# Performance work log

Measured on AMD Instinct MI355X. Metric: run time of the kernel, lower is better.

The kernel has to match this reference:

```python
import jax, jax.numpy as jnp
import numpy as np

N_NODES = 10000

def rgcn_layer(x, edge_index, basis, comp, root, bias):
    # x: [N, Fin]; edge_index: [R, 2, E] int; basis: [B, Fin, Fout]; comp: [R, B]
    R, _, E = edge_index.shape
    N = x.shape[0]
    src = edge_index[:, 0]  # [R, E]
    dst = edge_index[:, 1]  # [R, E]
    # basis-decomposed per-relation weights: W_r = sum_b comp[r,b] * basis[b]
    W = jnp.einsum('rb,bio->rio', comp, basis)          # [R, Fin, Fout]
    x_src = x[src]                                       # [R, E, Fin] gather
    msg = jnp.einsum('rei,rio->reo', x_src, W)           # [R, E, Fout]
    # per-relation mean aggregation onto destination nodes
    seg = (jnp.arange(R, dtype=dst.dtype)[:, None] * N + dst).reshape(-1)  # [R*E]
    agg = jax.ops.segment_sum(msg.reshape(R * E, -1), seg, num_segments=R * N)
    deg = jax.ops.segment_sum(jnp.ones((R * E,), x.dtype), seg, num_segments=R * N)
    agg = agg / jnp.maximum(deg, 1.0)[:, None]
    agg = agg.reshape(R, N, -1).sum(0)                   # sum over relations
    return agg + x @ root + bias


def setup_inputs() -> dict:
    key = jax.random.key(0)
    ks = jax.random.split(key, 10)
    s = 0.05  # scale params for numerical sanity
    return {
        'x_drug': jax.random.normal(ks[0], (N_NODES, 2048), jnp.float32),
        'drug_w': jax.random.normal(ks[1], (2048, 128), jnp.float32) * s,
        'edge_index': jax.random.randint(ks[2], (100, 2, 5000), 0, N_NODES, jnp.int32),
        'basis1': jax.random.normal(ks[3], (8, 128, 64), jnp.float32) * s,
        'comp1': jax.random.normal(ks[4], (100, 8), jnp.float32) * s,
        'root1': jax.random.normal(ks[5], (128, 64), jnp.float32) * s,
        'bias1': jnp.zeros((64,), jnp.float32),
        'basis2': jax.random.normal(ks[6], (8, 64, 20), jnp.float32) * s,
        'comp2': jax.random.normal(ks[7], (100, 8), jnp.float32) * s,
        'root2': jax.random.normal(ks[8], (64, 20), jnp.float32) * s,
        'bias2': jnp.zeros((20,), jnp.float32),
    }


def reference(x_drug, drug_w, edge_index, basis1, comp1, root1, bias1,
              basis2, comp2, root2, bias2):
    x = x_drug @ drug_w                                   # dense projection [N, 128]
    h = rgcn_layer(x, edge_index, basis1, comp1, root1, bias1)   # [N, 64]
    h = jax.nn.relu(h)
    out = rgcn_layer(h, edge_index, basis2, comp2, root2, bias2)  # [N, 20]
    return out
```

## Files before the change

### kernel.cpp

```cpp
#include <hip/hip_runtime.h>

#define NN 10000
#define RR 100
#define EE 5000
#define D0 2048
#define D1 128
#define D2 64
#define D3 20
#define NE (RR*EE)
#define MAXD 128

using short8  = __attribute__((ext_vector_type(8))) short;
using float4e = __attribute__((ext_vector_type(4))) float;

typedef const __attribute__((address_space(1))) void g_void;
typedef __attribute__((address_space(3))) void l_void;

__device__ __forceinline__ unsigned short f2bf(float f) {
  unsigned int u = __float_as_uint(f);
  unsigned int r = u + 0x7fffu + ((u >> 16) & 1u);
  return (unsigned short)(r >> 16);
}
__device__ __forceinline__ float bf2f(unsigned short u) {
  return __uint_as_float(((unsigned int)u) << 16);
}
__device__ __forceinline__ unsigned int pk2(float lo, float hi) {
  return ((unsigned int)f2bf(hi) << 16) | (unsigned int)f2bf(lo);
}

#define ZBLK 977
#define CURB 10
#define WTBLK 1024
#define W1BLK 288
#define W2BLK 72
__global__ __launch_bounds__(256) void prep_kernel(
    const float* __restrict__ W, const float* __restrict__ root1,
    const float* __restrict__ basis1, const float* __restrict__ root2,
    const float* __restrict__ basis2, int4* __restrict__ deg4,
    int4* __restrict__ cur4,
    unsigned short* __restrict__ Btw, unsigned short* __restrict__ Wc1T,
    unsigned short* __restrict__ Wc2T) {
  const int b = blockIdx.x, tid = threadIdx.x;
  if (b < ZBLK) {
    int i = b * 256 + tid;
    if (i < (NN * RR) / 4) deg4[i] = make_int4(0, 0, 0, 0);
  } else if (b < ZBLK + CURB) {
    int i = (b - ZBLK) * 256 + tid;
    if (i < 2504) cur4[i] = make_int4(0, 0, 0, 0);
  } else if (b < ZBLK + CURB + WTBLK) {
    int idx = (b - ZBLK - CURB) * 256 + tid;
    int n = idx >> 11, k = idx & 2047;
    Btw[idx] = f2bf(W[(size_t)k * 128 + n]);
  } else if (b < ZBLK + CURB + WTBLK + W1BLK) {
    int idx = (b - ZBLK - CURB - WTBLK) * 256 + tid;
    int o = idx / 1152, j = idx - o * 1152;
    float v = (j < 128) ? root1[j * 64 + o] : basis1[(j - 128) * 64 + o];
    Wc1T[idx] = f2bf(v);
  } else {
    int idx = (b - ZBLK - CURB - WTBLK - W1BLK) * 256 + tid;
    int c = idx / 576, j = idx - c * 576;
    float v = 0.f;
    if (c < 20) v = (j < 64) ? root2[j * 20 + c] : basis2[(j - 64) * 20 + c];
    Wc2T[idx] = f2bf(v);
  }
}

__global__ void deg_kernel(const int* __restrict__ ei, int* __restrict__ deg) {
  int gid = blockIdx.x * 256 + threadIdx.x;
  if (gid >= NE) return;
  int r = gid / EE, e = gid - r * EE;
  int d = ei[r * 2 * EE + EE + e];
  atomicAdd(&deg[r * NN + d], 1);
}

__global__ void scatter_kernel(const int* __restrict__ ei,
                               const int* __restrict__ deg,
                               int* __restrict__ cur, int* __restrict__ rec,
                               float* __restrict__ esc) {
  int gid = blockIdx.x * 256 + threadIdx.x;
  if (gid >= NE) return;
  int r = gid / EE, e = gid - r * EE;
  int s = ei[r * 2 * EE + e];
  int d = ei[r * 2 * EE + EE + e];
  int p = atomicAdd(&cur[d], 1);
  if (p < MAXD) {
    rec[d * MAXD + p] = (r << 14) | s;
    esc[d * MAXD + p] = 1.0f / fmaxf((float)deg[r * NN + d], 1.0f);
  }
}

__global__ __launch_bounds__(256) void gemm0_mfma(
    const float* __restrict__ A, const unsigned short* __restrict__ Btw,
    float* __restrict__ xp) {
  __shared__ __align__(16) unsigned short Asb[2][32 * 64];
  __shared__ __align__(16) unsigned short Bsb[2][128 * 64];
  const int tid = threadIdx.x;
  const int m0 = blockIdx.x * 32;
  const int ks = blockIdx.y;
  const int wv = tid >> 6, lane = tid & 63;
  const int lrow = lane & 15, quad = lane >> 4;
  const int mt = wv >> 1;
  const int nh = (wv & 1) * 4;

  const int ar = tid >> 3, ag = tid & 7;
  int gra = m0 + ar; if (gra >= NN) gra = NN - 1;
  const float* Ap = &A[(size_t)gra * D0 + ks * 512 + ag * 4];
  const int asw = (ar & 7) << 4;
  const int aw0 = (ar * 128 + ((ag * 8) ^ asw)) >> 1;
  const int aw1 = (ar * 128 + ((64 + ag * 8) ^ asw)) >> 1;

  const int rowB = wv * 32 + (lane >> 3);
  const int gch  = (lane & 7) ^ (lane >> 3);
  const unsigned short* BgBase = &Btw[(size_t)rowB * D0 + ks * 512 + gch * 8];
  const int ldsB = wv * 2048;

  float4 a0, a1;

#define G0_LOADB(buf, c)                                                     \
  { _Pragma("unroll")                                                        \
    for (int i = 0; i < 4; i++) {                                            \
      __builtin_amdgcn_global_load_lds(                                      \
          (g_void*)(BgBase + (size_t)i * 8 * D0 + (c) * 64),                 \
          (l_void*)&Bsb[buf][ldsB + i * 512], 16, 0, 0);                     \
    } }

#define G0_LOADA(c)                                  \
  { a0 = *(const float4*)(Ap + (c) * 64);            \
    a1 = *(const float4*)(Ap + (c) * 64 + 32); }

#define G0_STOREA(buf)                                                  \
  { uint2 p0, p1;                                                       \
    p0.x = pk2(a0.x, a0.y); p0.y = pk2(a0.z, a0.w);                     \
    p1.x = pk2(a1.x, a1.y); p1.y = pk2(a1.z, a1.w);                     \
    *(uint2*)&Asb[buf][aw0] = p0;                                       \
    *(uint2*)&Asb[buf][aw1] = p1; }

#define G0_COMPUTE(buf)                                                 \
  { const int arow = mt * 16 + lrow;                                    \
    const int aswz = (arow & 7) << 4;                                   \
    _Pragma("unroll")                                                   \
    for (int kk = 0; kk < 2; kk++) {                                    \
      short8 af = *(const short8*)&Asb[buf][(arow * 128 + ((quad * 16 + kk * 64) ^ aswz)) >> 1]; \
      _Pragma("unroll")                                                 \
      for (int nt = 0; nt < 4; nt++) {                                  \
        const int brow = (nh + nt) * 16 + lrow;                         \
        short8 bfr = *(const short8*)&Bsb[buf][(brow * 128 + ((quad * 16 + kk * 64) ^ ((brow & 7) << 4))) >> 1]; \
        acc[nt] = __builtin_amdgcn_mfma_f32_16x16x32_bf16(af, bfr, acc[nt], 0, 0, 0); \
      }                                                                 \
    } }

  float4e acc[4];
#pragma unroll
  for (int i = 0; i < 4; i++) { acc[i][0]=0.f; acc[i][1]=0.f; acc[i][2]=0.f; acc[i][3]=0.f; }

  G0_LOADB(0, 0);
  G0_LOADA(0);
  G0_STOREA(0);
  __syncthreads();

#pragma unroll
  for (int c = 0; c < 8; c++) {
    if (c < 7) {
      G0_LOADB((c + 1) & 1, c + 1);
      G0_LOADA(c + 1);
      __builtin_amdgcn_sched_barrier(0);
    }
    G0_COMPUTE(c & 1);
    if (c < 7) G0_STOREA((c + 1) & 1);
    __syncthreads();
  }

#pragma unroll
  for (int nt = 0; nt < 4; nt++) {
    const int col = (nh + nt) * 16 + lrow;
#pragma unroll
    for (int r = 0; r < 4; r++) {
      const int row = m0 + mt * 16 + quad * 4 + r;
      if (row < NN)
        xp[(size_t)ks * (NN * D1) + (size_t)row * D1 + col] = acc[nt][r];
    }
  }
}

__global__ void reduce_kernel(const float* __restrict__ xp,
                              unsigned short* __restrict__ xb) {
  int idx = (blockIdx.x * 256 + threadIdx.x) * 4;
  if (idx >= NN * D1) return;
  float4 a = *(const float4*)&xp[idx];
  float4 b = *(const float4*)&xp[NN * D1 + idx];
  float4 c = *(const float4*)&xp[2 * NN * D1 + idx];
  float4 d = *(const float4*)&xp[3 * NN * D1 + idx];
  ushort4 o;
  o.x = f2bf(a.x + b.x + c.x + d.x); o.y = f2bf(a.y + b.y + c.y + d.y);
  o.z = f2bf(a.z + b.z + c.z + d.z); o.w = f2bf(a.w + b.w + c.w + d.w);
  *(ushort4*)&xb[idx] = o;
}

__global__ __launch_bounds__(256) void agg1e_kernel(
    const unsigned short* __restrict__ xb, const int* __restrict__ cur,
    const int* __restrict__ rec, const float* __restrict__ esc,
    const float* __restrict__ comp, unsigned short* __restrict__ A1b) {
  __shared__ float s_comp[RR * 8];
  const int tid = threadIdx.x;
  for (int i = tid; i < RR * 8; i += 256) s_comp[i] = comp[i];
  __syncthreads();
  const int wv = tid >> 6, lane = tid & 63;
  const int n = blockIdx.x * 4 + wv;
  if (n >= NN) return;
  float acc[8][2];
#pragma unroll
  for (int b = 0; b < 8; b++) { acc[b][0] = 0.f; acc[b][1] = 0.f; }
  int cnt = cur[n]; if (cnt > MAXD) cnt = MAXD;
  const int beg = n * MAXD, end = beg + cnt;
  int idx = beg;
  for (; idx + 3 < end; idx += 4) {
    int rc[4]; float sc[4]; unsigned int xv[4];
#pragma unroll
    for (int u = 0; u < 4; u++) {
      rc[u] = rec[idx + u];
      sc[u] = esc[idx + u];
    }
#pragma unroll
    for (int u = 0; u < 4; u++)
      xv[u] = *(const unsigned int*)&xb[(size_t)(rc[u] & 16383) * D1 + lane * 2];
#pragma unroll
    for (int u = 0; u < 4; u++) {
      const float* cb = &s_comp[(rc[u] >> 14) * 8];
      float x0 = __uint_as_float((xv[u] & 0xffffu) << 16);
      float x1 = __uint_as_float(xv[u] & 0xffff0000u);
#pragma unroll
      for (int b = 0; b < 8; b++) {
        float w = sc[u] * cb[b];
        acc[b][0] += w * x0;
        acc[b][1] += w * x1;
      }
    }
  }
  for (; idx < end; idx++) {
    int rc = rec[idx];
    float sc = esc[idx];
    unsigned int xv = *(const unsigned int*)&xb[(size_t)(rc & 16383) * D1 + lane * 2];
    const float* cb = &s_comp[(rc >> 14) * 8];
    float x0 = __uint_as_float((xv & 0xffffu) << 16);
    float x1 = __uint_as_float(xv & 0xffff0000u);
#pragma unroll
    for (int b = 0; b < 8; b++) {
      float w = sc * cb[b];
      acc[b][0] += w * x0;
      acc[b][1] += w * x1;
    }
  }
#pragma unroll
  for (int b = 0; b < 8; b++) {
    ushort2 o; o.x = f2bf(acc[b][0]); o.y = f2bf(acc[b][1]);
    *(ushort2*)&A1b[(size_t)n * 1024 + b * 128 + lane * 2] = o;
  }
}

__global__ __launch_bounds__(256) void agg2e_kernel(
    const unsigned short* __restrict__ hb, const int* __restrict__ cur,
    const int* __restrict__ rec, const float* __restrict__ esc,
    const float* __restrict__ comp, unsigned short* __restrict__ A2b) {
  __shared__ float s_comp[RR * 8];
  const int tid = threadIdx.x;
  for (int i = tid; i < RR * 8; i += 256) s_comp[i] = comp[i];
  __syncthreads();
  const int wv = tid >> 6, lane = tid & 63;
  const int n = blockIdx.x * 4 + wv;
  if (n >= NN) return;
  float acc[8];
#pragma unroll
  for (int b = 0; b < 8; b++) acc[b] = 0.f;
  int cnt = cur[n]; if (cnt > MAXD) cnt = MAXD;
  const int beg = n * MAXD, end = beg + cnt;
  int idx = beg;
  for (; idx + 3 < end; idx += 4) {
    int rc[4]; float sc[4]; float hv[4];
#pragma unroll
    for (int u = 0; u < 4; u++) {
      rc[u] = rec[idx + u];
      sc[u] = esc[idx + u];
    }
#pragma unroll
    for (int u = 0; u < 4; u++)
      hv[u] = bf2f(hb[(size_t)(rc[u] & 16383) * D2 + lane]);
#pragma unroll
    for (int u = 0; u < 4; u++) {
      const float* cb = &s_comp[(rc[u] >> 14) * 8];
#pragma unroll
      for (int b = 0; b < 8; b++) acc[b] += sc[u] * cb[b] * hv[u];
    }
  }
  for (; idx < end; idx++) {
    int rc = rec[idx];
    float sc = esc[idx];
    float hv = bf2f(hb[(size_t)(rc & 16383) * D2 + lane]);
    const float* cb = &s_comp[(rc >> 14) * 8];
#pragma unroll
    for (int b = 0; b < 8; b++) acc[b] += sc * cb[b] * hv;
  }
#pragma unroll
  for (int b = 0; b < 8; b++)
    A2b[(size_t)n * 512 + b * 64 + lane] = f2bf(acc[b]);
}

__global__ __launch_bounds__(256) void hlayer_mfma(
    const unsigned short* __restrict__ xb, const unsigned short* __restrict__ A1b,
    const unsigned short* __restrict__ Wt, const float* __restrict__ bias1,
    unsigned short* __restrict__ hb) {
  __shared__ __align__(16) unsigned short Asb[2][32 * 64];
  __shared__ __align__(16) unsigned short Bsb[2][64 * 64];
  const int tid = threadIdx.x;
  const int m0 = blockIdx.x * 32;
  const int wv = tid >> 6, lane = tid & 63;
  const int lrow = lane & 15, quad = lane >> 4;
  const int mt = wv >> 1, nb = wv & 1;

  const int ar = tid >> 3, ac = tid & 7;
  int gr = m0 + ar; if (gr >= NN) gr = NN - 1;
  const unsigned short* Ax = &xb[(size_t)gr * D1 + ac * 8];
  const unsigned short* Aa = &A1b[(size_t)gr * 1024 + ac * 8];
  const int asw = (ar & 7) << 4;
  const int aw = (ar * 128 + ((ac * 16) ^ asw)) >> 1;

  const int br = tid >> 2, bq = tid & 3;
  const unsigned short* Bp = &Wt[(size_t)br * 1152 + bq * 16];
  const int bsw = (br & 7) << 4;
  const int bw0 = (br * 128 + ((bq * 32) ^ bsw)) >> 1;
  const int bw1 = (br * 128 + ((bq * 32 + 16) ^ bsw)) >> 1;

  uint4 ra, rb0, rb1;

#define H_LOADG(c)                                                       \
  { int kb = (c) * 64;                                                   \
    ra  = (kb < 128) ? *(const uint4*)(Ax + kb)                          \
                     : *(const uint4*)(Aa + (kb - 128));                 \
    rb0 = *(const uint4*)(Bp + kb);                                      \
    rb1 = *(const uint4*)(Bp + kb + 8); }

#define H_STOREL(buf)                                                    \
  { *(uint4*)&Asb[buf][aw]  = ra;                                        \
    *(uint4*)&Bsb[buf][bw0] = rb0;                                       \
    *(uint4*)&Bsb[buf][bw1] = rb1; }

#define H_COMPUTE(buf)                                                   \
  { const int arow = mt * 16 + lrow;                                     \
    const int aswz = (arow & 7) << 4;                                    \
    _Pragma("unroll")                                                    \
    for (int kk = 0; kk < 2; kk++) {                                     \
      short8 af = *(const short8*)&Asb[buf][(arow * 128 + ((quad * 16 + kk * 64) ^ aswz)) >> 1]; \
      _Pragma("unroll")                                                  \
      for (int nt = 0; nt < 2; nt++) {                                   \
        const int brow = nb * 32 + nt * 16 + lrow;                       \
        short8 bfr = *(const short8*)&Bsb[buf][(brow * 128 + ((quad * 16 + kk * 64) ^ ((brow & 7) << 4))) >> 1]; \
        acc[nt] = __builtin_amdgcn_mfma_f32_16x16x32_bf16(af, bfr, acc[nt], 0, 0, 0); \
      }                                                                  \
    } }

  float4e acc[2];
#pragma unroll
  for (int i = 0; i < 2; i++) { acc[i][0]=0.f; acc[i][1]=0.f; acc[i][2]=0.f; acc[i][3]=0.f; }

  H_LOADG(0);
  H_STOREL(0);
  __syncthreads();

#pragma unroll
  for (int c = 0; c < 18; c++) {
    if (c < 17) {
      H_LOADG(c + 1);
      __builtin_amdgcn_sched_barrier(0);
    }
    H_COMPUTE(c & 1);
    if (c < 17) H_STOREL((c + 1) & 1);
    __syncthreads();
  }

#pragma unroll
  for (int nt = 0; nt < 2; nt++) {
    int col = nb * 32 + nt * 16 + lrow;
    float bv = bias1[col];
#pragma unroll
    for (int r = 0; r < 4; r++) {
      int row = m0 + mt * 16 + quad * 4 + r;
      if (row < NN)
        hb[(size_t)row * D2 + col] = f2bf(fmaxf(acc[nt][r] + bv, 0.f));
    }
  }
}

__global__ __launch_bounds__(256) void out_mfma(
    const unsigned short* __restrict__ hb, const unsigned short* __restrict__ A2b,
    const unsigned short* __restrict__ Wt, const float* __restrict__ bias2,
    float* __restrict__ out) {
  __shared__ __align__(16) unsigned short Asb[2][32 * 64];
  __shared__ __align__(16) unsigned short Bsb[2][32 * 64];
  const int tid = threadIdx.x;
  const int m0 = blockIdx.x * 32;
  const int wv = tid >> 6, lane = tid & 63;
  const int lrow = lane & 15, quad = lane >> 4;
  const int mt = wv >> 1, ntn = wv & 1;

  const int ar = tid >> 3, ac = tid & 7;
  int gr = m0 + ar; if (gr >= NN) gr = NN - 1;
  const unsigned short* Ah = &hb[(size_t)gr * D2 + ac * 8];
  const unsigned short* Aa = &A2b[(size_t)gr * 512 + ac * 8];
  const unsigned short* Bp = &Wt[(size_t)ar * 576 + ac * 8];
  const int asw = (ar & 7) << 4;
  const int aw = (ar * 128 + ((ac * 16) ^ asw)) >> 1;

  uint4 ra, rb;

#define O_LOADG(c)                                                       \
  { int kb = (c) * 64;                                                   \
    ra = (kb < 64) ? *(const uint4*)(Ah)                                 \
                   : *(const uint4*)(Aa + (kb - 64));                    \
    rb = *(const uint4*)(Bp + kb); }

#define O_STOREL(buf)                                                    \
  { *(uint4*)&Asb[buf][aw] = ra;                                         \
    *(uint4*)&Bsb[buf][aw] = rb; }

#define O_COMPUTE(buf)                                                   \
  { const int arow = mt * 16 + lrow;                                     \
    const int aswz = (arow & 7) << 4;                                    \
    const int brow = ntn * 16 + lrow;                                    \
    const int bswz = (brow & 7) << 4;                                    \
    _Pragma("unroll")                                                    \
    for (int kk = 0; kk < 2; kk++) {                                     \
      short8 af = *(const short8*)&Asb[buf][(arow * 128 + ((quad * 16 + kk * 64) ^ aswz)) >> 1]; \
      short8 bfr = *(const short8*)&Bsb[buf][(brow * 128 + ((quad * 16 + kk * 64) ^ bswz)) >> 1]; \
      acc = __builtin_amdgcn_mfma_f32_16x16x32_bf16(af, bfr, acc, 0, 0, 0); \
    } }

  float4e acc;
  acc[0]=0.f; acc[1]=0.f; acc[2]=0.f; acc[3]=0.f;

  O_LOADG(0);
  O_STOREL(0);
  __syncthreads();

#pragma unroll
  for (int c = 0; c < 9; c++) {
    if (c < 8) {
      O_LOADG(c + 1);
      __builtin_amdgcn_sched_barrier(0);
    }
    O_COMPUTE(c & 1);
    if (c < 8) O_STOREL((c + 1) & 1);
    __syncthreads();
  }

  int col = ntn * 16 + lrow;
  if (col < D3) {
    float bv = bias2[col];
#pragma unroll
    for (int r = 0; r < 4; r++) {
      int row = m0 + mt * 16 + quad * 4 + r;
      if (row < NN)
        out[(size_t)row * D3 + col] = acc[r] + bv;
    }
  }
}

extern "C" void kernel_launch(void* const* d_in, const int* in_sizes, int n_in,
                              void* d_out, int out_size, void* d_ws,
                              size_t ws_size, hipStream_t stream) {
  const float* x_drug = (const float*)d_in[0];
  const float* drug_w = (const float*)d_in[1];
  const int*   ei     = (const int*)d_in[2];
  const float* basis1 = (const float*)d_in[3];
  const float* comp1  = (const float*)d_in[4];
  const float* root1  = (const float*)d_in[5];
  const float* bias1  = (const float*)d_in[6];
  const float* basis2 = (const float*)d_in[7];
  const float* comp2  = (const float*)d_in[8];
  const float* root2  = (const float*)d_in[9];
  const float* bias2  = (const float*)d_in[10];
  float* out = (float*)d_out;

  float* ws = (float*)d_ws;
  int*   deg  = (int*)ws;
  int*   cur  = deg + 1000000;
  int*   rec  = cur + 10016;
  float* esc  = (float*)(rec + NN * MAXD);
  unsigned short* xb   = (unsigned short*)(esc + NN * MAXD);
  unsigned short* hb   = (unsigned short*)((float*)xb + 640000);
  unsigned short* Btw  = (unsigned short*)((float*)hb + 320000);
  unsigned short* Wc1T = (unsigned short*)((float*)Btw + 131072);
  unsigned short* Wc2T = (unsigned short*)((float*)Wc1T + 36864);
  float* R1 = (float*)Wc2T + 9216;
  float* xp = R1;
  unsigned short* A1b = (unsigned short*)R1;
  unsigned short* A2b = (unsigned short*)R1;

  prep_kernel<<<ZBLK + CURB + WTBLK + W1BLK + W2BLK, 256, 0, stream>>>(
      drug_w, root1, basis1, root2, basis2, (int4*)deg, (int4*)cur,
      Btw, Wc1T, Wc2T);

  deg_kernel<<<(NE + 255) / 256, 256, 0, stream>>>(ei, deg);
  scatter_kernel<<<(NE + 255) / 256, 256, 0, stream>>>(ei, deg, cur, rec, esc);

  gemm0_mfma<<<dim3(313, 4), 256, 0, stream>>>(x_drug, Btw, xp);
  reduce_kernel<<<(NN * D1 / 4 + 255) / 256, 256, 0, stream>>>(xp, xb);

  agg1e_kernel<<<(NN + 3) / 4, 256, 0, stream>>>(xb, cur, rec, esc, comp1, A1b);
  hlayer_mfma<<<(NN + 31) / 32, 256, 0, stream>>>(xb, A1b, Wc1T, bias1, hb);

  agg2e_kernel<<<(NN + 3) / 4, 256, 0, stream>>>(hb, cur, rec, esc, comp2, A2b);
  out_mfma<<<(NN + 31) / 32, 256, 0, stream>>>(hb, A2b, Wc2T, bias2, out);
}
```

Baseline: 174.6 us.

## Drop split-K in input projection GEMM and write bf16 directly

```diff
diff --git a/kernel.cpp b/kernel.cpp
--- a/kernel.cpp
+++ b/kernel.cpp
@@ -91,30 +91,24 @@
 
 __global__ __launch_bounds__(256) void gemm0_mfma(
     const float* __restrict__ A, const unsigned short* __restrict__ Btw,
-    float* __restrict__ xp) {
-  __shared__ __align__(16) unsigned short Asb[2][32 * 64];
+    unsigned short* __restrict__ xb) {
+  __shared__ __align__(16) unsigned short Asb[2][16 * 64];
   __shared__ __align__(16) unsigned short Bsb[2][128 * 64];
   const int tid = threadIdx.x;
-  const int m0 = blockIdx.x * 32;
-  const int ks = blockIdx.y;
+  const int m0 = blockIdx.x * 16;
   const int wv = tid >> 6, lane = tid & 63;
   const int lrow = lane & 15, quad = lane >> 4;
-  const int mt = wv >> 1;
-  const int nh = (wv & 1) * 4;
-
-  const int ar = tid >> 3, ag = tid & 7;
-  int gra = m0 + ar; if (gra >= NN) gra = NN - 1;
-  const float* Ap = &A[(size_t)gra * D0 + ks * 512 + ag * 4];
-  const int asw = (ar & 7) << 4;
-  const int aw0 = (ar * 128 + ((ag * 8) ^ asw)) >> 1;
-  const int aw1 = (ar * 128 + ((64 + ag * 8) ^ asw)) >> 1;
+
+  const int ar = tid >> 4, ag = tid & 15;
+  const float* Ap = &A[(size_t)(m0 + ar) * D0 + ag * 4];
+  const int aw = (ar * 128 + ((ag * 8) ^ ((ar & 7) << 4))) >> 1;
 
   const int rowB = wv * 32 + (lane >> 3);
   const int gch  = (lane & 7) ^ (lane >> 3);
-  const unsigned short* BgBase = &Btw[(size_t)rowB * D0 + ks * 512 + gch * 8];
+  const unsigned short* BgBase = &Btw[(size_t)rowB * D0 + gch * 8];
   const int ldsB = wv * 2048;
 
-  float4 a0, a1;
+  float4 a0;
 
 #define G0_LOADB(buf, c)                                                     \
   { _Pragma("unroll")                                                        \
@@ -124,76 +118,56 @@
           (l_void*)&Bsb[buf][ldsB + i * 512], 16, 0, 0);                     \
     } }
 
-#define G0_LOADA(c)                                  \
-  { a0 = *(const float4*)(Ap + (c) * 64);            \
-    a1 = *(const float4*)(Ap + (c) * 64 + 32); }
+#define G0_LOADA(c)  { a0 = *(const float4*)(Ap + (c) * 64); }
 
 #define G0_STOREA(buf)                                                  \
-  { uint2 p0, p1;                                                       \
+  { uint2 p0;                                                           \
     p0.x = pk2(a0.x, a0.y); p0.y = pk2(a0.z, a0.w);                     \
-    p1.x = pk2(a1.x, a1.y); p1.y = pk2(a1.z, a1.w);                     \
-    *(uint2*)&Asb[buf][aw0] = p0;                                       \
-    *(uint2*)&Asb[buf][aw1] = p1; }
+    *(uint2*)&Asb[buf][aw] = p0; }
 
 #define G0_COMPUTE(buf)                                                 \
-  { const int arow = mt * 16 + lrow;                                    \
-    const int aswz = (arow & 7) << 4;                                   \
+  { const int aswz = (lrow & 7) << 4;                                   \
     _Pragma("unroll")                                                   \
     for (int kk = 0; kk < 2; kk++) {                                    \
-      short8 af = *(const short8*)&Asb[buf][(arow * 128 + ((quad * 16 + kk * 64) ^ aswz)) >> 1]; \
+      short8 af = *(const short8*)&Asb[buf][(lrow * 128 + ((quad * 16 + kk * 64) ^ aswz)) >> 1]; \
       _Pragma("unroll")                                                 \
-      for (int nt = 0; nt < 4; nt++) {                                  \
-        const int brow = (nh + nt) * 16 + lrow;                         \
+      for (int nt = 0; nt < 2; nt++) {                                  \
+        const int brow = wv * 32 + nt * 16 + lrow;                      \
         short8 bfr = *(const short8*)&Bsb[buf][(brow * 128 + ((quad * 16 + kk * 64) ^ ((brow & 7) << 4))) >> 1]; \
         acc[nt] = __builtin_amdgcn_mfma_f32_16x16x32_bf16(af, bfr, acc[nt], 0, 0, 0); \
       }                                                                 \
     } }
 
-  float4e acc[4];
-#pragma unroll
-  for (int i = 0; i < 4; i++) { acc[i][0]=0.f; acc[i][1]=0.f; acc[i][2]=0.f; acc[i][3]=0.f; }
+  float4e acc[2];
+#pragma unroll
+  for (int i = 0; i < 2; i++) { acc[i][0]=0.f; acc[i][1]=0.f; acc[i][2]=0.f; acc[i][3]=0.f; }
 
   G0_LOADB(0, 0);
   G0_LOADA(0);
   G0_STOREA(0);
   __syncthreads();
 
-#pragma unroll
-  for (int c = 0; c < 8; c++) {
-    if (c < 7) {
+#pragma unroll 4
+  for (int c = 0; c < 32; c++) {
+    if (c < 31) {
       G0_LOADB((c + 1) & 1, c + 1);
       G0_LOADA(c + 1);
       __builtin_amdgcn_sched_barrier(0);
     }
     G0_COMPUTE(c & 1);
-    if (c < 7) G0_STOREA((c + 1) & 1);
+    if (c < 31) G0_STOREA((c + 1) & 1);
     __syncthreads();
   }
 
 #pragma unroll
-  for (int nt = 0; nt < 4; nt++) {
-    const int col = (nh + nt) * 16 + lrow;
+  for (int nt = 0; nt < 2; nt++) {
+    const int col = wv * 32 + nt * 16 + lrow;
 #pragma unroll
     for (int r = 0; r < 4; r++) {
-      const int row = m0 + mt * 16 + quad * 4 + r;
-      if (row < NN)
-        xp[(size_t)ks * (NN * D1) + (size_t)row * D1 + col] = acc[nt][r];
-    }
-  }
-}
-
-__global__ void reduce_kernel(const float* __restrict__ xp,
-                              unsigned short* __restrict__ xb) {
-  int idx = (blockIdx.x * 256 + threadIdx.x) * 4;
-  if (idx >= NN * D1) return;
-  float4 a = *(const float4*)&xp[idx];
-  float4 b = *(const float4*)&xp[NN * D1 + idx];
-  float4 c = *(const float4*)&xp[2 * NN * D1 + idx];
-  float4 d = *(const float4*)&xp[3 * NN * D1 + idx];
-  ushort4 o;
-  o.x = f2bf(a.x + b.x + c.x + d.x); o.y = f2bf(a.y + b.y + c.y + d.y);
-  o.z = f2bf(a.z + b.z + c.z + d.z); o.w = f2bf(a.w + b.w + c.w + d.w);
-  *(ushort4*)&xb[idx] = o;
+      const int row = m0 + quad * 4 + r;
+      xb[(size_t)row * D1 + col] = f2bf(acc[nt][r]);
+    }
+  }
 }
 
 __global__ __launch_bounds__(256) void agg1e_kernel(
@@ -490,7 +464,6 @@
   unsigned short* Wc1T = (unsigned short*)((float*)Btw + 131072);
   unsigned short* Wc2T = (unsigned short*)((float*)Wc1T + 36864);
   float* R1 = (float*)Wc2T + 9216;
-  float* xp = R1;
   unsigned short* A1b = (unsigned short*)R1;
   unsigned short* A2b = (unsigned short*)R1;
 
@@ -501,8 +474,7 @@
   deg_kernel<<<(NE + 255) / 256, 256, 0, stream>>>(ei, deg);
   scatter_kernel<<<(NE + 255) / 256, 256, 0, stream>>>(ei, deg, cur, rec, esc);
 
-  gemm0_mfma<<<dim3(313, 4), 256, 0, stream>>>(x_drug, Btw, xp);
-  reduce_kernel<<<(NN * D1 / 4 + 255) / 256, 256, 0, stream>>>(xp, xb);
+  gemm0_mfma<<<NN / 16, 256, 0, stream>>>(x_drug, Btw, xb);
 
   agg1e_kernel<<<(NN + 3) / 4, 256, 0, stream>>>(xb, cur, rec, esc, comp1, A1b);
   hlayer_mfma<<<(NN + 31) / 32, 256, 0, stream>>>(xb, A1b, Wc1T, bias1, hb);
```

Result: no change. 172.0 us (-1.5%).
